# Performance work log

Measured on AMD Instinct MI355X. Metric: run time of the kernel, lower is better.

The kernel has to match this reference:

```python
import jax, jax.numpy as jnp
import numpy as np
from jax import lax

H = 128


def _ema_scan(x):
    # x: [B, T, N, F] -> EMA along T: s_t = 0.9*s_{t-1} + 0.1*x_t
    xt = jnp.moveaxis(x, 1, 0)  # [T, B, N, F]

    def step(s, xi):
        s = s * 0.9 + xi * 0.1
        return s, s

    _, ys = lax.scan(step, jnp.zeros_like(xt[0]), xt)
    return jnp.moveaxis(ys, 0, 1)  # [B, T, N, F]


def setup_inputs() -> dict:
    key = jax.random.key(0)
    k1, k2, k3, k4, k5 = jax.random.split(key, 5)
    B, T, N = 4, 96, 512
    x = jax.random.normal(k1, (B, T, N, H), dtype=jnp.float32)
    s = 1.0 / np.sqrt(H)
    W_exp = jax.random.uniform(k2, (2 * H, H), jnp.float32, -s, s)
    b_exp = jax.random.uniform(k3, (2 * H,), jnp.float32, -s, s)
    W_con = jax.random.uniform(k4, (H, H), jnp.float32, -s, s)
    b_con = jax.random.uniform(k5, (H,), jnp.float32, -s, s)
    return {"spatial_temporal_representation": x, "W_exp": W_exp, "b_exp": b_exp,
            "W_con": W_con, "b_con": b_con}


def reference(spatial_temporal_representation, W_exp, b_exp, W_con, b_con):
    x = spatial_temporal_representation  # [B,T,N,H]
    expanded = jnp.einsum('btnh,oh->btno', x, W_exp) + b_exp  # [B,T,N,2H]
    state_primary, state_gating = jnp.split(expanded, 2, axis=-1)
    gated_activation = jax.nn.sigmoid(_ema_scan(state_gating))
    out = jnp.einsum('btnh,oh->btno', state_primary * gated_activation, W_con) + b_con
    return out
```

## Files before the change

### kernel.cpp

```cpp
#include <hip/hip_runtime.h>

#define B_DIM 4
#define T_DIM 96
#define N_DIM 512
#define H_DIM 128
#define NH    (N_DIM * H_DIM)

#define WS_WEXP  0
#define WS_WCON  32768
#define WS_L     49152
#define WS_TOTAL 58368

typedef __attribute__((ext_vector_type(8))) short short8;
typedef __attribute__((ext_vector_type(4))) float f32x4;

__device__ __forceinline__ unsigned short f2b_rh(float f) {
    union { float f; unsigned u; } c; c.f = f;
    return (unsigned short)((c.u + 0x8000u) >> 16);
}
__device__ __forceinline__ unsigned pack_bf16_2(float a, float b) {
    union { float f; unsigned u; } ca, cb; ca.f = a; cb.f = b;
    return __builtin_amdgcn_perm(cb.u + 0x8000u, ca.u + 0x8000u, 0x07060302u);
}
__device__ __forceinline__ float b2f(unsigned short s) {
    union { unsigned u; float f; } c; c.u = ((unsigned)s) << 16;
    return c.f;
}

extern "C" __global__ void prep_kernel(const float* __restrict__ Wexp,
                                       const float* __restrict__ Wcon,
                                       unsigned short* __restrict__ ws) {
    int i = blockIdx.x * 256 + threadIdx.x;
    if (i < 32768) {
        ws[WS_WEXP + i] = f2b_rh(Wexp[i]);
    } else if (i < 49152) {
        int j = i - 32768;
        ws[WS_WCON + j] = f2b_rh(Wcon[j]);
    } else if (i < WS_TOTAL) {
        int j = i - 49152;
        int t = j / 96, k = j - t * 96;
        float v = 0.0f;
        if (k <= t) v = 0.1f * __expf((float)(t - k) * -0.1053605157f);
        ws[WS_L + j] = f2b_rh(v);
    }
}

extern "C" __global__ __launch_bounds__(256, 3)
void mamba_fused(const float* __restrict__ x,
                 const unsigned short* __restrict__ ws,
                 const float* __restrict__ b_exp,
                 const float* __restrict__ b_con,
                 float* __restrict__ out)
{
    __shared__ __align__(16) unsigned short prim[T_DIM * 136];
    __shared__ __align__(16) unsigned short gpg[H_DIM * 104];

    const int tid  = threadIdx.x;
    const int wave = tid >> 6;
    const int lane = tid & 63;
    const int q    = lane >> 4;
    const int l16  = lane & 15;

    const int blk = blockIdx.x;
    const int n   = blk & (N_DIM - 1);
    const int b   = blk >> 9;

    const float* xg = x + ((size_t)b * T_DIM * N_DIM + (size_t)n) * H_DIM;

    short8 wf[4][4];
    float4 bias1[4];
    {
        const int obase = wave * 64;
        const unsigned short* wsW = ws + WS_WEXP;
        for (int ot = 0; ot < 4; ++ot) {
            const unsigned short* wrow = wsW + (size_t)(obase + ot * 16 + l16) * H_DIM + q * 8;
            for (int k0 = 0; k0 < 4; ++k0)
                wf[ot][k0] = *(const short8*)(wrow + k0 * 32);
            bias1[ot] = *(const float4*)(b_exp + obase + ot * 16 + q * 4);
        }
    }

    for (int mt = 0; mt < 6; ++mt) {
        const float* xrow = xg + (size_t)(mt * 16 + l16) * NH + q * 8;
        short8 bfr[4];
        for (int k0 = 0; k0 < 4; ++k0) {
            float4 v0 = *(const float4*)(xrow + k0 * 32);
            float4 v1 = *(const float4*)(xrow + k0 * 32 + 4);
            union { unsigned u[4]; short8 s; } p;
            p.u[0] = pack_bf16_2(v0.x, v0.y);
            p.u[1] = pack_bf16_2(v0.z, v0.w);
            p.u[2] = pack_bf16_2(v1.x, v1.y);
            p.u[3] = pack_bf16_2(v1.z, v1.w);
            bfr[k0] = p.s;
        }
        const int tcol = mt * 16 + l16;
        for (int ot = 0; ot < 4; ++ot) {
            f32x4 acc = {0.f, 0.f, 0.f, 0.f};
            for (int k0 = 0; k0 < 4; ++k0)
                acc = __builtin_amdgcn_mfma_f32_16x16x32_bf16(wf[ot][k0], bfr[k0], acc, 0, 0, 0);
            const int o = wave * 64 + ot * 16 + q * 4;
            float r0 = acc[0] + bias1[ot].x, r1 = acc[1] + bias1[ot].y;
            float r2 = acc[2] + bias1[ot].z, r3 = acc[3] + bias1[ot].w;
            if (wave < 2) {
                union { unsigned u[2]; ushort4 s; } pk;
                pk.u[0] = pack_bf16_2(r0, r1);
                pk.u[1] = pack_bf16_2(r2, r3);
                *(ushort4*)&prim[tcol * 136 + o] = pk.s;
            } else {
                const int g = o - 128;
                gpg[(g + 0) * 104 + tcol] = f2b_rh(r0);
                gpg[(g + 1) * 104 + tcol] = f2b_rh(r1);
                gpg[(g + 2) * 104 + tcol] = f2b_rh(r2);
                gpg[(g + 3) * 104 + tcol] = f2b_rh(r3);
            }
        }
    }
    __syncthreads();

    f32x4 eacc[2][6];
    for (int ht = 0; ht < 2; ++ht)
        for (int tt = 0; tt < 6; ++tt)
            eacc[ht][tt] = (f32x4){0.f, 0.f, 0.f, 0.f};
    {
        const unsigned short* wsL = ws + WS_L;
        for (int kf = 0; kf < 3; ++kf) {
            short8 af[2];
            for (int ht = 0; ht < 2; ++ht) {
                const int h = (wave * 2 + ht) * 16 + l16;
                af[ht] = *(const short8*)&gpg[h * 104 + kf * 32 + q * 8];
            }
            for (int tt = 0; tt < 6; ++tt) {
                short8 bf = *(const short8*)(wsL + (size_t)(tt * 16 + l16) * 96 + kf * 32 + q * 8);
                eacc[0][tt] = __builtin_amdgcn_mfma_f32_16x16x32_bf16(af[0], bf, eacc[0][tt], 0, 0, 0);
                eacc[1][tt] = __builtin_amdgcn_mfma_f32_16x16x32_bf16(af[1], bf, eacc[1][tt], 0, 0, 0);
            }
        }
    }

    short8 wc[2][4];
    float4 bias2[2];
    {
        const int obase = wave * 32;
        const unsigned short* wsW = ws + WS_WCON;
        for (int ot = 0; ot < 2; ++ot) {
            const unsigned short* wrow = wsW + (size_t)(obase + ot * 16 + l16) * H_DIM + q * 8;
            for (int k0 = 0; k0 < 4; ++k0)
                wc[ot][k0] = *(const short8*)(wrow + k0 * 32);
            bias2[ot] = *(const float4*)(b_con + obase + ot * 16 + q * 4);
        }
    }
    __syncthreads();

    for (int ht = 0; ht < 2; ++ht) {
        const int hb = (wave * 2 + ht) * 16 + q * 4;
        for (int tt = 0; tt < 6; ++tt) {
            const int t = tt * 16 + l16;
            ushort4 pv = *(const ushort4*)&prim[t * 136 + hb];
            f32x4 s = eacc[ht][tt];
            float sg0 = __fdividef(1.f, 1.f + __expf(-s[0]));
            float sg1 = __fdividef(1.f, 1.f + __expf(-s[1]));
            float sg2 = __fdividef(1.f, 1.f + __expf(-s[2]));
            float sg3 = __fdividef(1.f, 1.f + __expf(-s[3]));
            float p0 = b2f(pv.x) * sg0, p1 = b2f(pv.y) * sg1;
            float p2 = b2f(pv.z) * sg2, p3 = b2f(pv.w) * sg3;
            union { unsigned u[2]; ushort4 s; } pk;
            pk.u[0] = pack_bf16_2(p0, p1);
            pk.u[1] = pack_bf16_2(p2, p3);
            *(ushort4*)&gpg[t * 136 + hb] = pk.s;
        }
    }
    __syncthreads();

    float* og = out + ((size_t)b * T_DIM * N_DIM + (size_t)n) * H_DIM;
    for (int mt = 0; mt < 6; ++mt) {
        short8 bfr[4];
        const unsigned short* prow = &gpg[(mt * 16 + l16) * 136];
        for (int k0 = 0; k0 < 4; ++k0)
            bfr[k0] = *(const short8*)(prow + k0 * 32 + q * 8);
        const int t = mt * 16 + l16;
        for (int ot = 0; ot < 2; ++ot) {
            f32x4 acc = {0.f, 0.f, 0.f, 0.f};
            for (int k0 = 0; k0 < 4; ++k0)
                acc = __builtin_amdgcn_mfma_f32_16x16x32_bf16(wc[ot][k0], bfr[k0], acc, 0, 0, 0);
            const int o = wave * 32 + ot * 16 + q * 4;
            float4 v;
            v.x = acc[0] + bias2[ot].x;
            v.y = acc[1] + bias2[ot].y;
            v.z = acc[2] + bias2[ot].z;
            v.w = acc[3] + bias2[ot].w;
            *(float4*)(og + (size_t)t * NH + o) = v;
        }
    }
}

extern "C" void kernel_launch(void* const* d_in, const int* in_sizes, int n_in,
                              void* d_out, int out_size, void* d_ws, size_t ws_size,
                              hipStream_t stream) {
    const float* x     = (const float*)d_in[0];
    const float* W_exp = (const float*)d_in[1];
    const float* b_exp = (const float*)d_in[2];
    const float* W_con = (const float*)d_in[3];
    const float* b_con = (const float*)d_in[4];
    float* out = (float*)d_out;
    unsigned short* ws = (unsigned short*)d_ws;

    hipLaunchKernelGGL(prep_kernel, dim3(WS_TOTAL / 256), dim3(256), 0, stream,
                       W_exp, W_con, ws);
    hipLaunchKernelGGL(mamba_fused, dim3(B_DIM * N_DIM), dim3(256), 0, stream,
                       x, ws, b_exp, b_con, out);
}
```

Before: 230.5 us.

## Keep primary activations in registers, shrink LDS, skip zero triangular EMA blocks

Work is reassigned so each wave computes both the primary and gating outputs for its own 32-column h slice. The primary half now stays in registers instead of a dedicated LDS buffer, which roughly halves LDS use and lets launch bounds ask for 4 blocks per CU instead of 3. The EMA matmul skips the all-zero upper-triangular blocks of the decay matrix. One barrier is removed by having each wave read its gate fragments right after writing them. The cost is higher register pressure (primf and afr arrays), which could cause spills at the new occupancy target.

```diff
diff --git a/kernel.cpp b/kernel.cpp
--- a/kernel.cpp
+++ b/kernel.cpp
@@ -45,15 +45,14 @@
     }
 }
 
-extern "C" __global__ __launch_bounds__(256, 3)
+extern "C" __global__ __launch_bounds__(256, 4)
 void mamba_fused(const float* __restrict__ x,
                  const unsigned short* __restrict__ ws,
                  const float* __restrict__ b_exp,
                  const float* __restrict__ b_con,
                  float* __restrict__ out)
 {
-    __shared__ __align__(16) unsigned short prim[T_DIM * 136];
-    __shared__ __align__(16) unsigned short gpg[H_DIM * 104];
+    __shared__ __align__(16) unsigned short smem[13312];
 
     const int tid  = threadIdx.x;
     const int wave = tid >> 6;
@@ -70,16 +69,18 @@
     short8 wf[4][4];
     float4 bias1[4];
     {
-        const int obase = wave * 64;
         const unsigned short* wsW = ws + WS_WEXP;
         for (int ot = 0; ot < 4; ++ot) {
-            const unsigned short* wrow = wsW + (size_t)(obase + ot * 16 + l16) * H_DIM + q * 8;
+            const int orow = (ot < 2) ? (wave * 32 + ot * 16)
+                                      : (128 + wave * 32 + (ot - 2) * 16);
+            const unsigned short* wrow = wsW + (size_t)(orow + l16) * H_DIM + q * 8;
             for (int k0 = 0; k0 < 4; ++k0)
                 wf[ot][k0] = *(const short8*)(wrow + k0 * 32);
-            bias1[ot] = *(const float4*)(b_exp + obase + ot * 16 + q * 4);
-        }
-    }
-
+            bias1[ot] = *(const float4*)(b_exp + orow + q * 4);
+        }
+    }
+
+    ushort4 primf[2][6];
     for (int mt = 0; mt < 6; ++mt) {
         const float* xrow = xg + (size_t)(mt * 16 + l16) * NH + q * 8;
         short8 bfr[4];
@@ -98,22 +99,28 @@
             f32x4 acc = {0.f, 0.f, 0.f, 0.f};
             for (int k0 = 0; k0 < 4; ++k0)
                 acc = __builtin_amdgcn_mfma_f32_16x16x32_bf16(wf[ot][k0], bfr[k0], acc, 0, 0, 0);
-            const int o = wave * 64 + ot * 16 + q * 4;
             float r0 = acc[0] + bias1[ot].x, r1 = acc[1] + bias1[ot].y;
             float r2 = acc[2] + bias1[ot].z, r3 = acc[3] + bias1[ot].w;
-            if (wave < 2) {
+            if (ot < 2) {
                 union { unsigned u[2]; ushort4 s; } pk;
                 pk.u[0] = pack_bf16_2(r0, r1);
                 pk.u[1] = pack_bf16_2(r2, r3);
-                *(ushort4*)&prim[tcol * 136 + o] = pk.s;
+                primf[ot][mt] = pk.s;
             } else {
-                const int g = o - 128;
-                gpg[(g + 0) * 104 + tcol] = f2b_rh(r0);
-                gpg[(g + 1) * 104 + tcol] = f2b_rh(r1);
-                gpg[(g + 2) * 104 + tcol] = f2b_rh(r2);
-                gpg[(g + 3) * 104 + tcol] = f2b_rh(r3);
+                const int g0 = wave * 32 + (ot - 2) * 16 + q * 4;
+                smem[(g0 + 0) * 104 + tcol] = f2b_rh(r0);
+                smem[(g0 + 1) * 104 + tcol] = f2b_rh(r1);
+                smem[(g0 + 2) * 104 + tcol] = f2b_rh(r2);
+                smem[(g0 + 3) * 104 + tcol] = f2b_rh(r3);
             }
         }
+    }
+
+    short8 afr[2][3];
+    for (int ht = 0; ht < 2; ++ht) {
+        const int h = (wave * 2 + ht) * 16 + l16;
+        for (int kf = 0; kf < 3; ++kf)
+            afr[ht][kf] = *(const short8*)&smem[h * 104 + kf * 32 + q * 8];
     }
     __syncthreads();
 
@@ -124,57 +131,49 @@
     {
         const unsigned short* wsL = ws + WS_L;
         for (int kf = 0; kf < 3; ++kf) {
-            short8 af[2];
-            for (int ht = 0; ht < 2; ++ht) {
-                const int h = (wave * 2 + ht) * 16 + l16;
-                af[ht] = *(const short8*)&gpg[h * 104 + kf * 32 + q * 8];
+            for (int tt = 2 * kf; tt < 6; ++tt) {
+                short8 bf = *(const short8*)(wsL + (size_t)(tt * 16 + l16) * 96 + kf * 32 + q * 8);
+                eacc[0][tt] = __builtin_amdgcn_mfma_f32_16x16x32_bf16(afr[0][kf], bf, eacc[0][tt], 0, 0, 0);
+                eacc[1][tt] = __builtin_amdgcn_mfma_f32_16x16x32_bf16(afr[1][kf], bf, eacc[1][tt], 0, 0, 0);
             }
-            for (int tt = 0; tt < 6; ++tt) {
-                short8 bf = *(const short8*)(wsL + (size_t)(tt * 16 + l16) * 96 + kf * 32 + q * 8);
-                eacc[0][tt] = __builtin_amdgcn_mfma_f32_16x16x32_bf16(af[0], bf, eacc[0][tt], 0, 0, 0);
-                eacc[1][tt] = __builtin_amdgcn_mfma_f32_16x16x32_bf16(af[1], bf, eacc[1][tt], 0, 0, 0);
-            }
-        }
-    }
-
-    short8 wc[2][4];
-    float4 bias2[2];
-    {
-        const int obase = wave * 32;
-        const unsigned short* wsW = ws + WS_WCON;
-        for (int ot = 0; ot < 2; ++ot) {
-            const unsigned short* wrow = wsW + (size_t)(obase + ot * 16 + l16) * H_DIM + q * 8;
-            for (int k0 = 0; k0 < 4; ++k0)
-                wc[ot][k0] = *(const short8*)(wrow + k0 * 32);
-            bias2[ot] = *(const float4*)(b_con + obase + ot * 16 + q * 4);
-        }
-    }
-    __syncthreads();
+        }
+    }
 
     for (int ht = 0; ht < 2; ++ht) {
-        const int hb = (wave * 2 + ht) * 16 + q * 4;
+        const int hb = wave * 32 + ht * 16 + q * 4;
         for (int tt = 0; tt < 6; ++tt) {
             const int t = tt * 16 + l16;
-            ushort4 pv = *(const ushort4*)&prim[t * 136 + hb];
             f32x4 s = eacc[ht][tt];
             float sg0 = __fdividef(1.f, 1.f + __expf(-s[0]));
             float sg1 = __fdividef(1.f, 1.f + __expf(-s[1]));
             float sg2 = __fdividef(1.f, 1.f + __expf(-s[2]));
             float sg3 = __fdividef(1.f, 1.f + __expf(-s[3]));
+            ushort4 pv = primf[ht][tt];
             float p0 = b2f(pv.x) * sg0, p1 = b2f(pv.y) * sg1;
             float p2 = b2f(pv.z) * sg2, p3 = b2f(pv.w) * sg3;
             union { unsigned u[2]; ushort4 s; } pk;
             pk.u[0] = pack_bf16_2(p0, p1);
             pk.u[1] = pack_bf16_2(p2, p3);
-            *(ushort4*)&gpg[t * 136 + hb] = pk.s;
+            *(ushort4*)&smem[t * 136 + hb] = pk.s;
         }
     }
     __syncthreads();
 
+    short8 wc[2][4];
+    float4 bias2[2];
+    {
+        const unsigned short* wsW = ws + WS_WCON;
+        for (int ot = 0; ot < 2; ++ot) {
+            const unsigned short* wrow = wsW + (size_t)(wave * 32 + ot * 16 + l16) * H_DIM + q * 8;
+            for (int k0 = 0; k0 < 4; ++k0)
+                wc[ot][k0] = *(const short8*)(wrow + k0 * 32);
+            bias2[ot] = *(const float4*)(b_con + wave * 32 + ot * 16 + q * 4);
+        }
+    }
     float* og = out + ((size_t)b * T_DIM * N_DIM + (size_t)n) * H_DIM;
     for (int mt = 0; mt < 6; ++mt) {
         short8 bfr[4];
-        const unsigned short* prow = &gpg[(mt * 16 + l16) * 136];
+        const unsigned short* prow = &smem[(mt * 16 + l16) * 136];
         for (int k0 = 0; k0 < 4; ++k0)
             bfr[k0] = *(const short8*)(prow + k0 * 32 + q * 8);
         const int t = mt * 16 + l16;
```

Result: slower. 247.5 us (+7.4%).
